# Kernel tuning notes

Measured on AMD Instinct MI355X. Metric: run time of the kernel, lower is better.

Reference implementation:

```python
import jax, jax.numpy as jnp
import numpy as np
import math

T = 4096
HID = 2048
H = 16
D = 128
RD = 64            # rotary_dim = head_dim * partial_rotary_factor (0.5)
THETA = 10000.0
EPS = 1e-6
GROUPS = 8
LAYER_IDX = 2
N_LAYERS = 32


def build_slope_tensor(num_heads):
    def get_slopes_power_of_2(n):
        start = 2 ** (-(2 ** (-(math.log2(n) - 3))))
        ratio = start
        return [start * ratio ** i for i in range(n)]
    if math.log2(num_heads).is_integer():
        return get_slopes_power_of_2(num_heads)
    closest = 2 ** math.floor(math.log2(num_heads))
    return (get_slopes_power_of_2(closest)
            + build_slope_tensor(2 * closest)[0::2][: num_heads - closest])


def compute_slope():
    base = np.array(build_slope_tensor(H), dtype=np.float32)
    return jnp.asarray(-base * (1 - (LAYER_IDX - 1) / (N_LAYERS - 1) + 1e-5), dtype=jnp.float32)


def setup_inputs() -> dict:
    key = jax.random.key(0)
    ks = jax.random.split(key, 8)
    s = 0.02
    return {
        "positions": jnp.arange(T, dtype=jnp.int32),
        "hidden_states": jax.random.normal(ks[0], (T, HID), dtype=jnp.float32),
        "recurrent_state": jnp.zeros((1, H, D, D), dtype=jnp.float32),
        "w_qkv": jax.random.normal(ks[1], (HID, 3 * H * D), dtype=jnp.float32) * s,
        "w_g": jax.random.normal(ks[2], (HID, H * D), dtype=jnp.float32) * s,
        "w_dense": jax.random.normal(ks[3], (H * D, HID), dtype=jnp.float32) * s,
        "q_norm_w": jnp.ones((D,), dtype=jnp.float32),
        "k_norm_w": jnp.ones((D,), dtype=jnp.float32),
        "g_norm_w": jnp.ones((H * D,), dtype=jnp.float32),
    }


def _rms(x, w):
    var = jnp.mean(jnp.square(x), axis=-1, keepdims=True)
    return x * jax.lax.rsqrt(var + EPS) * w


def _rope(x, positions):
    # partial neox-style rotary on first RD dims of each head
    inv_freq = 1.0 / (THETA ** (jnp.arange(0, RD, 2, dtype=jnp.float32) / RD))
    freqs = positions.astype(jnp.float32)[:, None] * inv_freq   # [T, RD/2]
    cos = jnp.cos(freqs)[:, None, :]                            # [T, 1, RD/2]
    sin = jnp.sin(freqs)[:, None, :]
    x1 = x[..., : RD // 2]
    x2 = x[..., RD // 2 : RD]
    x_pass = x[..., RD:]
    return jnp.concatenate([x1 * cos - x2 * sin, x2 * cos + x1 * sin, x_pass], axis=-1)


def reference(positions, hidden_states, recurrent_state,
              w_qkv, w_g, w_dense, q_norm_w, k_norm_w, g_norm_w):
    t = hidden_states.shape[0]
    qkv = (hidden_states @ w_qkv).reshape(t, 3, H, D)
    q, k, v = qkv[:, 0], qkv[:, 1], qkv[:, 2]
    q = _rms(q, q_norm_w)
    k = _rms(k, k_norm_w)
    q = _rope(q, positions)
    k = _rope(k, positions)

    slope = compute_slope()                    # [H], negative
    decay = jnp.exp(slope)                     # per-head per-step decay
    scale = D ** -0.5
    q = (q * scale).astype(jnp.float32)
    k = k.astype(jnp.float32)
    v = v.astype(jnp.float32)

    def step(S, qkv_t):
        q_t, k_t, v_t = qkv_t                  # each [H, D]
        S = S * decay[:, None, None] + k_t[:, :, None] * v_t[:, None, :]
        o_t = jnp.einsum('hk,hkv->hv', q_t, S)
        return S, o_t

    S0 = recurrent_state[0].astype(jnp.float32)   # [H, K, V]
    S_final, o = jax.lax.scan(step, S0, (q, k, v))
    attn = o.reshape(t, H * D)

    gate = jax.nn.sigmoid(hidden_states @ w_g)
    # GroupRMSNorm: normalize per group of size (H*D)/GROUPS, scale by full weight
    g = attn.reshape(t, GROUPS, (H * D) // GROUPS)
    var = jnp.mean(jnp.square(g), axis=-1, keepdims=True)
    g = (g * jax.lax.rsqrt(var + EPS)).reshape(t, H * D) * g_norm_w

    out = (g * gate) @ w_dense
    return out, S_final[None]
```

## Files before the change

### kernel.cpp

```cpp
#include <hip/hip_runtime.h>
#include <hip/hip_bf16.h>

using bf16x8 = __attribute__((ext_vector_type(8))) __bf16;
using f32x4  = __attribute__((ext_vector_type(4))) float;

constexpr int T_SEQ = 4096;
constexpr int HID_C = 2048;
constexpr int NH    = 16;
constexpr int QKV_N = 6144;

__device__ __forceinline__ float head_slope(int h) {
    return -exp2f(-0.5f * (float)(h + 1)) * 0.967751935483871f;
}

__device__ __forceinline__ ushort f2bfu(float f) {
    __hip_bfloat16 h = __float2bfloat16(f);
    return *(ushort*)&h;
}
__device__ __forceinline__ float bfu2f(ushort u) {
    union { unsigned int i; float f; } x; x.i = ((unsigned int)u) << 16; return x.f;
}

__device__ __forceinline__ void async16(const ushort* g, ushort* l) {
    __builtin_amdgcn_global_load_lds((const __attribute__((address_space(1))) void*)g,
                                     (__attribute__((address_space(3))) void*)l, 16, 0, 0);
}

__global__ __launch_bounds__(256) void cvt_bf16(const float* __restrict__ src,
                                                ushort* __restrict__ dst, int n) {
    int i = (blockIdx.x * 256 + threadIdx.x) * 8;
    if (i >= n) return;
    float4 a = *(const float4*)(src + i);
    float4 b = *(const float4*)(src + i + 4);
    ushort4 ua = {f2bfu(a.x), f2bfu(a.y), f2bfu(a.z), f2bfu(a.w)};
    ushort4 ub = {f2bfu(b.x), f2bfu(b.y), f2bfu(b.z), f2bfu(b.w)};
    *(ushort4*)(dst + i) = ua;
    *(ushort4*)(dst + i + 4) = ub;
}

__global__ __launch_bounds__(256) void transpose_cvt(const float* __restrict__ src,
                                                     ushort* __restrict__ dst,
                                                     int R, int C) {
    __shared__ ushort tile[64][68];
    int t = threadIdx.x;
    int tr = blockIdx.y * 64, tc = blockIdx.x * 64;
    int r0 = t >> 4;
    int c4 = (t & 15) << 2;
#pragma unroll
    for (int p = 0; p < 4; ++p) {
        int row = r0 + p * 16;
        float4 v = *(const float4*)&src[(size_t)(tr + row) * C + tc + c4];
        tile[row][c4 + 0] = f2bfu(v.x);
        tile[row][c4 + 1] = f2bfu(v.y);
        tile[row][c4 + 2] = f2bfu(v.z);
        tile[row][c4 + 3] = f2bfu(v.w);
    }
    __syncthreads();
#pragma unroll
    for (int p = 0; p < 4; ++p) {
        int orow = r0 + p * 16;
        ushort4 u;
        u.x = tile[c4 + 0][orow];
        u.y = tile[c4 + 1][orow];
        u.z = tile[c4 + 2][orow];
        u.w = tile[c4 + 3][orow];
        *(ushort4*)&dst[(size_t)(tc + orow) * R + tr + c4] = u;
    }
}

__device__ __forceinline__ void gemm8_core(const ushort* __restrict__ Ag,
                                           const ushort* __restrict__ Bg,
                                           int K, int bm, int bn,
                                           ushort* sh, f32x4 (&acc)[8][4]) {
    const int tid  = threadIdx.x;
    const int lane = tid & 63;
    const int wave = tid >> 6;
    const int lane15 = lane & 15, quad = lane >> 4;
    const int wm = wave >> 2, wn = wave & 3;
    const int swz = lane15 & 7;

    ushort* const ldsA0 = sh;
    ushort* const ldsA1 = sh + 16384;
    ushort* const ldsB0 = sh + 32768;
    ushort* const ldsB1 = sh + 49152;

    const int srow = lane >> 3;
    const int scol = ((lane & 7) ^ srow) << 3;
    const ushort* gA = Ag + (size_t)(bm + srow) * K + scol;
    const ushort* gB = Bg + (size_t)(bn + srow) * K + scol;
    const int ro = wave * 16;
    const int NT = K >> 6;

#define ST_A(L, h, k0) do { \
    async16(gA + (size_t)((h) * 128 + ro) * K + (k0),     (L) + ((h) * 128 + ro) * 64); \
    async16(gA + (size_t)((h) * 128 + ro + 8) * K + (k0), (L) + ((h) * 128 + ro + 8) * 64); } while (0)
#define ST_B(L, h, k0) do { \
    async16(gB + (size_t)((h) * 128 + ro) * K + (k0),     (L) + ((h) * 128 + ro) * 64); \
    async16(gB + (size_t)((h) * 128 + ro + 8) * K + (k0), (L) + ((h) * 128 + ro + 8) * 64); } while (0)
#define RD_A(L, p) do { \
    _Pragma("unroll") for (int m2 = 0; m2 < 2; ++m2) \
    _Pragma("unroll") for (int ks = 0; ks < 2; ++ks) \
        afr[m2][ks] = *(const bf16x8*)&(L)[(wm * 128 + ((p) * 2 + m2) * 16 + lane15) * 64 + (((ks * 4 + quad) ^ swz) << 3)]; } while (0)
#define RD_B(L) do { \
    _Pragma("unroll") for (int j = 0; j < 4; ++j) \
    _Pragma("unroll") for (int ks = 0; ks < 2; ++ks) \
        bfr[j][ks] = *(const bf16x8*)&(L)[(wn * 64 + j * 16 + lane15) * 64 + (((ks * 4 + quad) ^ swz) << 3)]; } while (0)
#define MFMA_PH(p) do { \
    asm volatile("s_barrier" ::: "memory"); \
    asm volatile("s_waitcnt lgkmcnt(0)" ::: "memory"); \
    __builtin_amdgcn_s_setprio(1); \
    _Pragma("unroll") for (int m2 = 0; m2 < 2; ++m2) \
    _Pragma("unroll") for (int j = 0; j < 4; ++j) \
    _Pragma("unroll") for (int ks = 0; ks < 2; ++ks) \
        acc[(p) * 2 + m2][j] = __builtin_amdgcn_mfma_f32_16x16x32_bf16(afr[m2][ks], bfr[j][ks], acc[(p) * 2 + m2][j], 0, 0, 0); \
    __builtin_amdgcn_s_setprio(0); } while (0)
#define KTILE(LAc, LBc, LAn, LBn, t) do { \
    const int k0 = (t) << 6; \
    bf16x8 bfr[4][2]; \
    bf16x8 afr[2][2]; \
    RD_B(LBc); RD_A(LAc, 0); \
    if ((t) + 1 < NT) ST_A(LAn, 0, k0 + 64); \
    MFMA_PH(0); \
    asm volatile("s_barrier" ::: "memory"); \
    RD_A(LAc, 1); \
    if ((t) + 1 < NT) ST_A(LAn, 1, k0 + 64); \
    MFMA_PH(1); \
    asm volatile("s_barrier" ::: "memory"); \
    RD_A(LAc, 2); \
    if ((t) + 2 < NT) ST_B(LBc, 0, k0 + 128); \
    MFMA_PH(2); \
    asm volatile("s_barrier" ::: "memory"); \
    RD_A(LAc, 3); \
    if ((t) + 2 < NT) ST_B(LBc, 1, k0 + 128); \
    MFMA_PH(3); \
    if ((t) + 2 < NT) { asm volatile("s_waitcnt vmcnt(4)" ::: "memory"); } \
    else              { asm volatile("s_waitcnt vmcnt(0)" ::: "memory"); } \
    asm volatile("s_barrier" ::: "memory"); } while (0)

    ST_A(ldsA0, 0, 0); ST_A(ldsA0, 1, 0);
    ST_B(ldsB0, 0, 0); ST_B(ldsB0, 1, 0);
    ST_B(ldsB1, 0, 64); ST_B(ldsB1, 1, 64);
    asm volatile("s_waitcnt vmcnt(4)" ::: "memory");
    asm volatile("s_barrier" ::: "memory");

    for (int t = 0; t < NT; t += 2) {
        KTILE(ldsA0, ldsB0, ldsA1, ldsB1, t);
        KTILE(ldsA1, ldsB1, ldsA0, ldsB0, t + 1);
    }
#undef ST_A
#undef ST_B
#undef RD_A
#undef RD_B
#undef MFMA_PH
#undef KTILE
}

__global__ __launch_bounds__(512, 2) void gemm_fused(const ushort* __restrict__ A,
                                                     const ushort* __restrict__ Bcat,
                                                     ushort* __restrict__ qkv,
                                                     ushort* __restrict__ gate, int K) {
    __shared__ ushort sh[65536];
    int nwg = gridDim.x;
    int bid = blockIdx.x;
    int swzb = (bid & 7) * (nwg >> 3) + (bid >> 3);
    int GN = (QKV_N + HID_C) >> 8;
    int bn = (swzb % GN) * 256;
    int bm = (swzb / GN) * 256;
    f32x4 acc[8][4] = {};
    gemm8_core(A, Bcat, K, bm, bn, sh, acc);

    int lane = threadIdx.x & 63, wave = threadIdx.x >> 6;
    int lane15 = lane & 15, quad = lane >> 4;
    int wm = wave >> 2, wn = wave & 3;
    bool isg = bn >= QKV_N;
    ushort* outp = isg ? gate : qkv;
    int ncol = isg ? HID_C : QKV_N;
    int cb = (isg ? bn - QKV_N : bn) + wn * 64;
    int rb = bm + wm * 128;
#pragma unroll
    for (int i = 0; i < 8; ++i)
#pragma unroll
        for (int j = 0; j < 4; ++j) {
            int col = cb + j * 16 + lane15;
#pragma unroll
            for (int r = 0; r < 4; ++r) {
                float v = acc[i][j][r];
                if (isg) v = 1.0f / (1.0f + __expf(-v));
                outp[(size_t)(rb + i * 16 + quad * 4 + r) * ncol + col] = f2bfu(v);
            }
        }
}

__global__ __launch_bounds__(512, 2) void gemm_dense(const ushort* __restrict__ A,
                                                     const ushort* __restrict__ Bt,
                                                     float* __restrict__ Cout, int N, int K) {
    __shared__ ushort sh[65536];
    int nwg = gridDim.x;
    int bid = blockIdx.x;
    int swzb = (bid & 7) * (nwg >> 3) + (bid >> 3);
    int GN = N >> 8;
    int bn = (swzb % GN) * 256;
    int bm = (swzb / GN) * 256;
    f32x4 acc[8][4] = {};
    gemm8_core(A, Bt, K, bm, bn, sh, acc);

    int lane = threadIdx.x & 63, wave = threadIdx.x >> 6;
    int lane15 = lane & 15, quad = lane >> 4;
    int wm = wave >> 2, wn = wave & 3;
    int cb = bn + wn * 64;
    int rb = bm + wm * 128;
#pragma unroll
    for (int i = 0; i < 8; ++i)
#pragma unroll
        for (int j = 0; j < 4; ++j) {
            int col = cb + j * 16 + lane15;
#pragma unroll
            for (int r = 0; r < 4; ++r)
                Cout[(size_t)(rb + i * 16 + quad * 4 + r) * N + col] = acc[i][j][r];
        }
}

__global__ __launch_bounds__(256) void rope_tab(const int* __restrict__ positions,
                                                float2* __restrict__ tab) {
    int i = blockIdx.x * 256 + threadIdx.x;
    int t = i >> 5, fi = i & 31;
    float inv = expf((float)fi * -0.2878231366f);
    float freq = (float)positions[t] * inv;
    float sn, cs;
    sincosf(freq, &sn, &cs);
    tab[i] = make_float2(cs, sn);
}

__global__ __launch_bounds__(256) void qk_rope_T(ushort* __restrict__ qkv,
                                                 const float2* __restrict__ tab,
                                                 const float* __restrict__ qw,
                                                 const float* __restrict__ kw,
                                                 ushort* __restrict__ kT,
                                                 ushort* __restrict__ vT) {
    __shared__ ushort tile[64][132];
    int bt = blockIdx.x;
    int kind = blockIdx.y >> 4, h = blockIdx.y & 15;
    int tid = threadIdx.x;
    int row = tid >> 2, c = tid & 3, d0 = c * 32;
    int t = bt * 64 + row;
    ushort* base = qkv + (size_t)t * QKV_N + kind * 2048 + h * 128 + d0;
    bf16x8 pk[4];
#pragma unroll
    for (int p = 0; p < 4; ++p) pk[p] = *(const bf16x8*)(base + p * 8);
    if (kind < 2) {
        float x[32];
        float ss = 0.f;
#pragma unroll
        for (int p = 0; p < 4; ++p)
#pragma unroll
            for (int i = 0; i < 8; ++i) {
                x[p * 8 + i] = (float)pk[p][i];
                ss += x[p * 8 + i] * x[p * 8 + i];
            }
        ss += __shfl_xor(ss, 1);
        ss += __shfl_xor(ss, 2);
        float rr = rsqrtf(ss * (1.0f / 128.0f) + 1e-6f);
        const float* w = (kind == 0) ? qw : kw;
#pragma unroll
        for (int i = 0; i < 32; ++i) x[i] *= rr * w[d0 + i];
#pragma unroll
        for (int i = 0; i < 32; ++i) {
            float p = __shfl_xor(x[i], 1);
            if (c < 2) {
                float2 rt = tab[t * 32 + i];
                x[i] = (c == 0) ? (x[i] * rt.x - p * rt.y) : (x[i] * rt.x + p * rt.y);
            }
        }
        float sc = (kind == 0) ? 0.08838834764831845f : 1.0f;
#pragma unroll
        for (int p = 0; p < 4; ++p)
#pragma unroll
            for (int i = 0; i < 8; ++i) pk[p][i] = (__bf16)(x[p * 8 + i] * sc);
#pragma unroll
        for (int p = 0; p < 4; ++p) *(bf16x8*)(base + p * 8) = pk[p];
    }
    if (kind >= 1) {
#pragma unroll
        for (int p = 0; p < 4; ++p) {
            ushort4* s = (ushort4*)&pk[p];
            *(ushort4*)&tile[row][d0 + p * 8]     = s[0];
            *(ushort4*)&tile[row][d0 + p * 8 + 4] = s[1];
        }
        __syncthreads();
        ushort* outT = ((kind == 1) ? kT : vT) + (size_t)(h * 128) * T_SEQ + bt * 64;
        int d = tid >> 1, half = tid & 1;
#pragma unroll
        for (int tt = 0; tt < 8; ++tt) {
            int tl = half * 32 + tt * 4;
            ushort4 u;
            u.x = tile[tl + 0][d];
            u.y = tile[tl + 1][d];
            u.z = tile[tl + 2][d];
            u.w = tile[tl + 3][d];
            *(ushort4*)&outT[(size_t)d * T_SEQ + tl] = u;
        }
    }
}

__global__ __launch_bounds__(256) void chunk_partial(const ushort* __restrict__ kT,
                                                     const ushort* __restrict__ vT,
                                                     float* __restrict__ PT) {
    int c = blockIdx.x, h = blockIdx.y;
    float slope = head_slope(h);
    float lam_inv = __expf(-slope);
    int tid = threadIdx.x, lane = tid & 63, wave = tid >> 6;
    int lane15 = lane & 15, quad = lane >> 4;
    int wv = (wave & 1) * 64, wd = (wave >> 1) * 64;
    const ushort* vbase = vT + (size_t)h * 128 * T_SEQ + c * 128;
    const ushort* kbase = kT + (size_t)h * 128 * T_SEQ + c * 128;
    f32x4 acc[4][4] = {};
#pragma unroll
    for (int j0 = 0; j0 < 128; j0 += 32) {
        float w8[8];
        w8[0] = __expf(slope * (float)(127 - (j0 + quad * 8)));
#pragma unroll
        for (int kk = 1; kk < 8; ++kk) w8[kk] = w8[kk - 1] * lam_inv;
        bf16x8 afr[4], bfr[4];
#pragma unroll
        for (int i = 0; i < 4; ++i) {
            bf16x8 v = *(const bf16x8*)&vbase[(size_t)(wv + i * 16 + lane15) * T_SEQ + j0 + quad * 8];
#pragma unroll
            for (int kk = 0; kk < 8; ++kk) afr[i][kk] = (__bf16)((float)v[kk] * w8[kk]);
        }
#pragma unroll
        for (int j = 0; j < 4; ++j)
            bfr[j] = *(const bf16x8*)&kbase[(size_t)(wd + j * 16 + lane15) * T_SEQ + j0 + quad * 8];
#pragma unroll
        for (int i = 0; i < 4; ++i)
#pragma unroll
            for (int j = 0; j < 4; ++j)
                acc[i][j] = __builtin_amdgcn_mfma_f32_16x16x32_bf16(afr[i], bfr[j], acc[i][j], 0, 0, 0);
    }
    float* out = PT + ((size_t)c * 16 + h) * 16384;
#pragma unroll
    for (int i = 0; i < 4; ++i)
#pragma unroll
        for (int j = 0; j < 4; ++j)
#pragma unroll
            for (int r = 0; r < 4; ++r)
                out[(size_t)(wv + i * 16 + quad * 4 + r) * 128 + wd + j * 16 + lane15] = acc[i][j][r];
}

__global__ __launch_bounds__(128) void scan_states(const float* __restrict__ PT,
                                                   const float* __restrict__ S0,
                                                   ushort* __restrict__ Spb,
                                                   float* __restrict__ Sfin) {
    int hv = blockIdx.x;
    int d = threadIdx.x;
    int h = hv >> 7, v = hv & 127;
    float lamC = __expf(head_slope(h) * 128.0f);
    float s = S0[(size_t)h * 16384 + d * 128 + v];
#pragma unroll
    for (int c = 0; c < 32; ++c) {
        size_t idx = ((size_t)c * 2048 + hv) * 128 + d;
        Spb[idx] = f2bfu(s);
        s = s * lamC + PT[idx];
    }
    Sfin[(size_t)h * 16384 + d * 128 + v] = s;
}

__global__ __launch_bounds__(256) void chunk_out(const ushort* __restrict__ qkv,
                                                 const ushort* __restrict__ vT,
                                                 const ushort* __restrict__ Spb,
                                                 ushort* __restrict__ o) {
    int c = blockIdx.x, h = blockIdx.y;
    float slope = head_slope(h);
    __shared__ ushort Ps[128 * 136];
    int tid = threadIdx.x, lane = tid & 63, wave = tid >> 6;
    int lane15 = lane & 15, quad = lane >> 4;
    int t0 = c * 128;
    int tt0 = wave, tt1 = 7 - wave;
    const ushort* qbase = qkv + (size_t)t0 * QKV_N + h * 128;
    const ushort* kbase = qbase + 2048;

    bf16x8 qf0[4], qf1[4];
#pragma unroll
    for (int ds = 0; ds < 4; ++ds) {
        qf0[ds] = *(const bf16x8*)&qbase[(size_t)(tt0 * 16 + lane15) * QKV_N + ds * 32 + quad * 8];
        qf1[ds] = *(const bf16x8*)&qbase[(size_t)(tt1 * 16 + lane15) * QKV_N + ds * 32 + quad * 8];
    }
    f32x4 s0a[4] = {};
    f32x4 s1a[8] = {};
#pragma unroll
    for (int st = 0; st < 8; ++st) {
        if (st <= tt1) {
            bf16x8 kf[4];
#pragma unroll
            for (int ds = 0; ds < 4; ++ds)
                kf[ds] = *(const bf16x8*)&kbase[(size_t)(st * 16 + lane15) * QKV_N + ds * 32 + quad * 8];
#pragma unroll
            for (int ds = 0; ds < 4; ++ds)
                s1a[st] = __builtin_amdgcn_mfma_f32_16x16x32_bf16(qf1[ds], kf[ds], s1a[st], 0, 0, 0);
            if (st <= tt0) {
#pragma unroll
                for (int ds = 0; ds < 4; ++ds)
                    s0a[st] = __builtin_amdgcn_mfma_f32_16x16x32_bf16(qf0[ds], kf[ds], s0a[st], 0, 0, 0);
            }
        }
    }
    int stmax0 = tt0 + ((tt0 & 1) ? 0 : 1);
    int stmax1 = tt1 + ((tt1 & 1) ? 0 : 1);
#pragma unroll
    for (int st = 0; st < 8; ++st) {
        if (st <= stmax1) {
#pragma unroll
            for (int r = 0; r < 4; ++r) {
                int t = tt1 * 16 + quad * 4 + r;
                int s = st * 16 + lane15;
                float val = 0.f;
                if (st <= tt1) val = (s <= t) ? s1a[st][r] * __expf(slope * (float)(t - s)) : 0.f;
                Ps[t * 136 + s] = f2bfu(val);
            }
        }
    }
#pragma unroll
    for (int st = 0; st < 5; ++st) {
        if (st <= stmax0) {
#pragma unroll
            for (int r = 0; r < 4; ++r) {
                int t = tt0 * 16 + quad * 4 + r;
                int s = st * 16 + lane15;
                float val = 0.f;
                if (st <= tt0) val = (s <= t) ? s0a[st][r] * __expf(slope * (float)(t - s)) : 0.f;
                Ps[t * 136 + s] = f2bfu(val);
            }
        }
    }
    __syncthreads();
    f32x4 oa0[8] = {};
    f32x4 oa1[8] = {};
    float lam0 = __expf(slope * (float)(tt0 * 16 + lane15 + 1));
    float lam1 = __expf(slope * (float)(tt1 * 16 + lane15 + 1));
    bf16x8 qs0[4], qs1[4];
#pragma unroll
    for (int ds = 0; ds < 4; ++ds)
#pragma unroll
        for (int kk = 0; kk < 8; ++kk) {
            qs0[ds][kk] = (__bf16)((float)qf0[ds][kk] * lam0);
            qs1[ds][kk] = (__bf16)((float)qf1[ds][kk] * lam1);
        }
    const ushort* spb = Spb + ((size_t)c * 2048 + h * 128) * 128;
#pragma unroll
    for (int vt = 0; vt < 8; ++vt)
#pragma unroll
        for (int ds = 0; ds < 4; ++ds) {
            bf16x8 bfrag = *(const bf16x8*)&spb[(vt * 16 + lane15) * 128 + ds * 32 + quad * 8];
            oa0[vt] = __builtin_amdgcn_mfma_f32_16x16x32_bf16(qs0[ds], bfrag, oa0[vt], 0, 0, 0);
            oa1[vt] = __builtin_amdgcn_mfma_f32_16x16x32_bf16(qs1[ds], bfrag, oa1[vt], 0, 0, 0);
        }
    const ushort* vbase = vT + (size_t)h * 128 * T_SEQ + t0;
    int ns0 = (tt0 + 2) >> 1, ns1 = (tt1 + 2) >> 1;
#pragma unroll
    for (int s32 = 0; s32 < 4; ++s32) {
        if (s32 < ns1) {
            bf16x8 af = *(const bf16x8*)&Ps[(tt1 * 16 + lane15) * 136 + s32 * 32 + quad * 8];
#pragma unroll
            for (int vt = 0; vt < 8; ++vt) {
                bf16x8 bfrag = *(const bf16x8*)&vbase[(size_t)(vt * 16 + lane15) * T_SEQ + s32 * 32 + quad * 8];
                oa1[vt] = __builtin_amdgcn_mfma_f32_16x16x32_bf16(af, bfrag, oa1[vt], 0, 0, 0);
            }
        }
    }
#pragma unroll
    for (int s32 = 0; s32 < 2; ++s32) {
        if (s32 < ns0) {
            bf16x8 af = *(const bf16x8*)&Ps[(tt0 * 16 + lane15) * 136 + s32 * 32 + quad * 8];
#pragma unroll
            for (int vt = 0; vt < 8; ++vt) {
                bf16x8 bfrag = *(const bf16x8*)&vbase[(size_t)(vt * 16 + lane15) * T_SEQ + s32 * 32 + quad * 8];
                oa0[vt] = __builtin_amdgcn_mfma_f32_16x16x32_bf16(af, bfrag, oa0[vt], 0, 0, 0);
            }
        }
    }
#pragma unroll
    for (int vt = 0; vt < 8; ++vt)
#pragma unroll
        for (int r = 0; r < 4; ++r) {
            o[(size_t)(t0 + tt0 * 16 + quad * 4 + r) * 2048 + h * 128 + vt * 16 + lane15] = f2bfu(oa0[vt][r]);
            o[(size_t)(t0 + tt1 * 16 + quad * 4 + r) * 2048 + h * 128 + vt * 16 + lane15] = f2bfu(oa1[vt][r]);
        }
}

__global__ __launch_bounds__(256) void gnorm_gate(const ushort* __restrict__ o,
                                                  const ushort* __restrict__ gate,
                                                  const float* __restrict__ gw,
                                                  ushort* __restrict__ gg) {
    int t = blockIdx.x;
    int tid = threadIdx.x;
    const ushort* op = o + (size_t)t * 2048 + tid * 8;
    bf16x8 xv = *(const bf16x8*)op;
    float x[8];
    float ss = 0.0f;
#pragma unroll
    for (int i = 0; i < 8; ++i) { x[i] = (float)xv[i]; ss += x[i] * x[i]; }
#pragma unroll
    for (int off = 16; off > 0; off >>= 1) ss += __shfl_xor(ss, off);
    float r = rsqrtf(ss * (1.0f / 256.0f) + 1e-6f);
    const ushort* gp = gate + (size_t)t * 2048;
#pragma unroll
    for (int i = 0; i < 8; ++i) {
        int j = tid * 8 + i;
        float val = x[i] * r * gw[j] * bfu2f(gp[j]);
        gg[(size_t)t * 2048 + j] = f2bfu(val);
    }
}

extern "C" void kernel_launch(void* const* d_in, const int* in_sizes, int n_in,
                              void* d_out, int out_size, void* d_ws, size_t ws_size,
                              hipStream_t stream) {
    const int* positions   = (const int*)d_in[0];
    const float* hidden    = (const float*)d_in[1];
    const float* S0        = (const float*)d_in[2];
    const float* w_qkv     = (const float*)d_in[3];
    const float* w_g       = (const float*)d_in[4];
    const float* w_dense   = (const float*)d_in[5];
    const float* qw        = (const float*)d_in[6];
    const float* kw        = (const float*)d_in[7];
    const float* gw        = (const float*)d_in[8];

    char* ws = (char*)d_ws;
    ushort* qkv     = (ushort*)ws;
    ushort* wqkv_t  = (ushort*)(ws + 50331648);
    ushort* wg_t    = (ushort*)(ws + 75497472);
    float2* ropet   = (float2*)(ws + 50331648);
    float*  PT      = (float*)(ws + 50331648);
    ushort* wd_t    = (ushort*)(ws + 83886080);
    ushort* gatebuf = (ushort*)(ws + 92274688);
    ushort* hid_b   = (ushort*)(ws + 109051904);
    ushort* Spb     = (ushort*)(ws + 109051904);
    ushort* kT      = (ushort*)(ws + 125829120);
    ushort* vT      = (ushort*)(ws + 142606336);
    ushort* gg      = (ushort*)ws;

    float* out  = (float*)d_out;
    float* Sfin = out + (size_t)T_SEQ * HID_C;
    ushort* obuf = (ushort*)d_out;

    cvt_bf16<<<T_SEQ * HID_C / (256 * 8), 256, 0, stream>>>(hidden, hid_b, T_SEQ * HID_C);
    transpose_cvt<<<dim3(QKV_N / 64, HID_C / 64), 256, 0, stream>>>(w_qkv, wqkv_t, HID_C, QKV_N);
    transpose_cvt<<<dim3(HID_C / 64, HID_C / 64), 256, 0, stream>>>(w_g, wg_t, HID_C, HID_C);
    transpose_cvt<<<dim3(HID_C / 64, HID_C / 64), 256, 0, stream>>>(w_dense, wd_t, HID_C, HID_C);

    gemm_fused<<<dim3(512), 512, 0, stream>>>(hid_b, wqkv_t, qkv, gatebuf, HID_C);

    rope_tab<<<T_SEQ * 32 / 256, 256, 0, stream>>>(positions, ropet);
    qk_rope_T<<<dim3(T_SEQ / 64, 48), 256, 0, stream>>>(qkv, ropet, qw, kw, kT, vT);

    chunk_partial<<<dim3(32, 16), 256, 0, stream>>>(kT, vT, PT);
    scan_states<<<2048, 128, 0, stream>>>(PT, S0, Spb, Sfin);
    chunk_out<<<dim3(32, 16), 256, 0, stream>>>(qkv, vT, Spb, obuf);
    gnorm_gate<<<T_SEQ, 256, 0, stream>>>(obuf, gatebuf, gw, gg);

    gemm_dense<<<dim3(128), 512, 0, stream>>>(gg, wd_t, out, HID_C, HID_C);
}
```

Before: 467.5 us.

## Templatize GEMM core tile shape; use 256x128 tiles for dense GEMM

The shared GEMM core becomes a template over per-wave M fragments and B tile width, so the dense output projection can use 256x128 tiles and launch 256 workgroups instead of 128. The aim is better coverage of the device's compute units on the small final GEMM, plus smaller shared memory per block. Both GEMMs also switch to a new grid-to-tile mapping that groups workgroups into regions for cache locality. The cost is lower per-tile reuse and more B loads relative to compute in the dense GEMM.

```diff
diff --git a/kernel.cpp b/kernel.cpp
--- a/kernel.cpp
+++ b/kernel.cpp
@@ -24,6 +24,13 @@
 __device__ __forceinline__ void async16(const ushort* g, ushort* l) {
     __builtin_amdgcn_global_load_lds((const __attribute__((address_space(1))) void*)g,
                                      (__attribute__((address_space(3))) void*)l, 16, 0, 0);
+}
+
+template<int N> __device__ __forceinline__ void waitcnt_vm() {
+    if constexpr (N == 0)      asm volatile("s_waitcnt vmcnt(0)" ::: "memory");
+    else if constexpr (N == 2) asm volatile("s_waitcnt vmcnt(2)" ::: "memory");
+    else if constexpr (N == 4) asm volatile("s_waitcnt vmcnt(4)" ::: "memory");
+    else if constexpr (N == 6) asm volatile("s_waitcnt vmcnt(6)" ::: "memory");
 }
 
 __global__ __launch_bounds__(256) void cvt_bf16(const float* __restrict__ src,
@@ -68,39 +75,46 @@
     }
 }
 
+template<int MI, int BN>
 __device__ __forceinline__ void gemm8_core(const ushort* __restrict__ Ag,
                                            const ushort* __restrict__ Bg,
                                            int K, int bm, int bn,
-                                           ushort* sh, f32x4 (&acc)[8][4]) {
+                                           ushort* sh, f32x4 (&acc)[MI][4]) {
+    constexpr int WM = 16 / MI;
+    constexpr int WN = 8 / WM;
+    constexpr int MP = MI / 4;
+    constexpr int SB = BN / 128;
+
     const int tid  = threadIdx.x;
     const int lane = tid & 63;
     const int wave = tid >> 6;
     const int lane15 = lane & 15, quad = lane >> 4;
-    const int wm = wave >> 2, wn = wave & 3;
+    const int wm = wave / WN, wn = wave % WN;
     const int swz = lane15 & 7;
 
     ushort* const ldsA0 = sh;
     ushort* const ldsA1 = sh + 16384;
     ushort* const ldsB0 = sh + 32768;
-    ushort* const ldsB1 = sh + 49152;
+    ushort* const ldsB1 = sh + 32768 + BN * 64;
 
     const int srow = lane >> 3;
     const int scol = ((lane & 7) ^ srow) << 3;
     const ushort* gA = Ag + (size_t)(bm + srow) * K + scol;
     const ushort* gB = Bg + (size_t)(bn + srow) * K + scol;
-    const int ro = wave * 16;
+    const int ro  = wave * 16;
+    const int roB = wave * 8 * SB;
     const int NT = K >> 6;
 
 #define ST_A(L, h, k0) do { \
-    async16(gA + (size_t)((h) * 128 + ro) * K + (k0),     (L) + ((h) * 128 + ro) * 64); \
-    async16(gA + (size_t)((h) * 128 + ro + 8) * K + (k0), (L) + ((h) * 128 + ro + 8) * 64); } while (0)
+    _Pragma("unroll") for (int q = 0; q < 2; ++q) \
+        async16(gA + (size_t)((h) * 128 + ro + q * 8) * K + (k0), (L) + ((h) * 128 + ro + q * 8) * 64); } while (0)
 #define ST_B(L, h, k0) do { \
-    async16(gB + (size_t)((h) * 128 + ro) * K + (k0),     (L) + ((h) * 128 + ro) * 64); \
-    async16(gB + (size_t)((h) * 128 + ro + 8) * K + (k0), (L) + ((h) * 128 + ro + 8) * 64); } while (0)
+    _Pragma("unroll") for (int q = 0; q < SB; ++q) \
+        async16(gB + (size_t)((h) * (BN / 2) + roB + q * 8) * K + (k0), (L) + ((h) * (BN / 2) + roB + q * 8) * 64); } while (0)
 #define RD_A(L, p) do { \
-    _Pragma("unroll") for (int m2 = 0; m2 < 2; ++m2) \
+    _Pragma("unroll") for (int m2 = 0; m2 < MP; ++m2) \
     _Pragma("unroll") for (int ks = 0; ks < 2; ++ks) \
-        afr[m2][ks] = *(const bf16x8*)&(L)[(wm * 128 + ((p) * 2 + m2) * 16 + lane15) * 64 + (((ks * 4 + quad) ^ swz) << 3)]; } while (0)
+        afr[m2][ks] = *(const bf16x8*)&(L)[(wm * (MI * 16) + ((p) * MP + m2) * 16 + lane15) * 64 + (((ks * 4 + quad) ^ swz) << 3)]; } while (0)
 #define RD_B(L) do { \
     _Pragma("unroll") for (int j = 0; j < 4; ++j) \
     _Pragma("unroll") for (int ks = 0; ks < 2; ++ks) \
@@ -109,15 +123,15 @@
     asm volatile("s_barrier" ::: "memory"); \
     asm volatile("s_waitcnt lgkmcnt(0)" ::: "memory"); \
     __builtin_amdgcn_s_setprio(1); \
-    _Pragma("unroll") for (int m2 = 0; m2 < 2; ++m2) \
+    _Pragma("unroll") for (int m2 = 0; m2 < MP; ++m2) \
     _Pragma("unroll") for (int j = 0; j < 4; ++j) \
     _Pragma("unroll") for (int ks = 0; ks < 2; ++ks) \
-        acc[(p) * 2 + m2][j] = __builtin_amdgcn_mfma_f32_16x16x32_bf16(afr[m2][ks], bfr[j][ks], acc[(p) * 2 + m2][j], 0, 0, 0); \
+        acc[(p) * MP + m2][j] = __builtin_amdgcn_mfma_f32_16x16x32_bf16(afr[m2][ks], bfr[j][ks], acc[(p) * MP + m2][j], 0, 0, 0); \
     __builtin_amdgcn_s_setprio(0); } while (0)
 #define KTILE(LAc, LBc, LAn, LBn, t) do { \
     const int k0 = (t) << 6; \
     bf16x8 bfr[4][2]; \
-    bf16x8 afr[2][2]; \
+    bf16x8 afr[MP][2]; \
     RD_B(LBc); RD_A(LAc, 0); \
     if ((t) + 1 < NT) ST_A(LAn, 0, k0 + 64); \
     MFMA_PH(0); \
@@ -133,14 +147,14 @@
     RD_A(LAc, 3); \
     if ((t) + 2 < NT) ST_B(LBc, 1, k0 + 128); \
     MFMA_PH(3); \
-    if ((t) + 2 < NT) { asm volatile("s_waitcnt vmcnt(4)" ::: "memory"); } \
-    else              { asm volatile("s_waitcnt vmcnt(0)" ::: "memory"); } \
+    if ((t) + 2 < NT) { waitcnt_vm<2 * SB>(); } \
+    else              { waitcnt_vm<0>(); } \
     asm volatile("s_barrier" ::: "memory"); } while (0)
 
     ST_A(ldsA0, 0, 0); ST_A(ldsA0, 1, 0);
     ST_B(ldsB0, 0, 0); ST_B(ldsB0, 1, 0);
     ST_B(ldsB1, 0, 64); ST_B(ldsB1, 1, 64);
-    asm volatile("s_waitcnt vmcnt(4)" ::: "memory");
+    waitcnt_vm<2 * SB>();
     asm volatile("s_barrier" ::: "memory");
 
     for (int t = 0; t < NT; t += 2) {
@@ -160,14 +174,14 @@
                                                      ushort* __restrict__ qkv,
                                                      ushort* __restrict__ gate, int K) {
     __shared__ ushort sh[65536];
-    int nwg = gridDim.x;
     int bid = blockIdx.x;
-    int swzb = (bid & 7) * (nwg >> 3) + (bid >> 3);
-    int GN = (QKV_N + HID_C) >> 8;
-    int bn = (swzb % GN) * 256;
-    int bm = (swzb / GN) * 256;
+    int x = bid & 7, w = bid >> 3;
+    int rm = x >> 2, rn = x & 3;
+    int wm_i = w >> 3, wn_i = w & 7;
+    int bm = (rm * 8 + wm_i) * 256;
+    int bn = (rn * 8 + wn_i) * 256;
     f32x4 acc[8][4] = {};
-    gemm8_core(A, Bcat, K, bm, bn, sh, acc);
+    gemm8_core<8, 256>(A, Bcat, K, bm, bn, sh, acc);
 
     int lane = threadIdx.x & 63, wave = threadIdx.x >> 6;
     int lane15 = lane & 15, quad = lane >> 4;
@@ -194,23 +208,23 @@
 __global__ __launch_bounds__(512, 2) void gemm_dense(const ushort* __restrict__ A,
                                                      const ushort* __restrict__ Bt,
                                                      float* __restrict__ Cout, int N, int K) {
-    __shared__ ushort sh[65536];
-    int nwg = gridDim.x;
+    __shared__ ushort sh[49152];
     int bid = blockIdx.x;
-    int swzb = (bid & 7) * (nwg >> 3) + (bid >> 3);
-    int GN = N >> 8;
-    int bn = (swzb % GN) * 256;
-    int bm = (swzb / GN) * 256;
-    f32x4 acc[8][4] = {};
-    gemm8_core(A, Bt, K, bm, bn, sh, acc);
+    int x = bid & 7, w = bid >> 3;
+    int rm = x >> 1, rn = x & 1;
+    int wm_i = w >> 3, wn_i = w & 7;
+    int bm = (rm * 4 + wm_i) * 256;
+    int bn = (rn * 8 + wn_i) * 128;
+    f32x4 acc[4][4] = {};
+    gemm8_core<4, 128>(A, Bt, K, bm, bn, sh, acc);
 
     int lane = threadIdx.x & 63, wave = threadIdx.x >> 6;
     int lane15 = lane & 15, quad = lane >> 4;
-    int wm = wave >> 2, wn = wave & 3;
+    int wm = wave >> 1, wn = wave & 1;
     int cb = bn + wn * 64;
-    int rb = bm + wm * 128;
-#pragma unroll
-    for (int i = 0; i < 8; ++i)
+    int rb = bm + wm * 64;
+#pragma unroll
+    for (int i = 0; i < 4; ++i)
 #pragma unroll
         for (int j = 0; j < 4; ++j) {
             int col = cb + j * 16 + lane15;
@@ -556,5 +570,5 @@
     chunk_out<<<dim3(32, 16), 256, 0, stream>>>(qkv, vT, Spb, obuf);
     gnorm_gate<<<T_SEQ, 256, 0, stream>>>(obuf, gatebuf, gw, gg);
 
-    gemm_dense<<<dim3(128), 512, 0, stream>>>(gg, wd_t, out, HID_C, HID_C);
-}
+    gemm_dense<<<dim3(256), 512, 0, stream>>>(gg, wd_t, out, HID_C, HID_C);
+}
```

Result: faster. 446.5 us (-4.5%).
